# Performance work log

Hardware: AMD Instinct MI355X
Metric: run time of the kernel (lower is better)

## Reference

```python
import jax, jax.numpy as jnp
import numpy as np

B, G, S, GS, P = 32, 512, 128, 32, 10
C, H, RED = 384, 6, 16
HID = 4 * C
D = C // H
SCALE = D ** -0.5

def _gelu(x):
    return jax.nn.gelu(x, approximate=False)

def _ln(x, g, b):
    m = jnp.mean(x, -1, keepdims=True)
    v = jnp.var(x, -1, keepdims=True)
    return (x - m) * jax.lax.rsqrt(v + 1e-5) * g + b

def _split_qkv(x, W):
    Bn, T, Cc = x.shape
    qkv = (x @ W).reshape(Bn, T, 3, H, D).transpose(2, 0, 3, 1, 4)
    return qkv[0], qkv[1], qkv[2]

def _merge(x):
    Bn, Hh, T, Dd = x.shape
    return x.transpose(0, 2, 1, 3).reshape(Bn, T, Hh * Dd)

def _mha(q, k, v):
    a = jax.nn.softmax(jnp.einsum('bhnd,bhmd->bhnm', q, k) * SCALE, axis=-1)
    return jnp.einsum('bhnm,bhmd->bhnd', a, v)

def _forward(x, center1, center2, neighborhood, prompt_embeddings, ln1_g, ln1_b, Wqkv, Wproj, bproj, gate, ln2_g, ln2_b, W1, b1, W2, b2, ad_down_W, ad_down_b, ad_up_W, ad_up_b, ad_gate, bn_g, bn_b, bn_mean, bn_var, ln3_g, ln3_b, a1_Wqkv, a1_Wproj, a1_bproj, ad1_down_W, ad1_down_b, ad1_up_W, ad1_up_b, idx, center_idx, group_size, if_maxmean, pro_cof, center_cof):
    Bx, Ntok, Cc = x.shape
    # prompt dropout is identity in eval
    prompt = jnp.broadcast_to(prompt_embeddings, (Bx, P, Cc))
    # --- gated dual self / prompt-cross attention ---
    xn = _ln(x, ln1_g, ln1_b)
    q, k, v = _split_qkv(xn, Wqkv)
    xs = _mha(q, k, v)                                  # [B,H,N,D]
    _, pk, pv = _split_qkv(prompt, Wqkv)
    pa = jax.nn.softmax(jnp.einsum('bhnd,bhpd->bhnp', q, pk) * SCALE, axis=-1)
    px = jnp.einsum('bhnp,bhpd->bhnd', gate * pa, pv)   # learned gate per head
    x = x + (_merge(xs) + _merge(px)) @ Wproj + bproj
    # --- MLP + gated bottleneck adapter residual ---
    h = _gelu(_ln(x, ln2_g, ln2_b) @ W1 + b1) @ W2 + b2
    h_ad = h + _gelu(h @ ad_down_W + ad_down_b) @ ad_up_W + ad_up_b
    x = ad_gate * h_ad + x
    cls_x = x[:, :1]
    xt = x[:, 1:]                                       # [B,G,C]
    flat = xt.reshape(Bx * G, Cc)
    x_nb = flat[idx].reshape(Bx * S, group_size, Cc)    # KNN neighborhoods
    x_ct = flat[center_idx].reshape(Bx, S, Cc)          # center features
    # NOTE: original normalizes `neighborhood` by its std, but result is unused
    # --- local self-attention (attn1 over norm3) on each neighborhood ---
    nq, nk, nv = _split_qkv(_ln(x_nb, ln3_g, ln3_b), a1_Wqkv)
    no = _mha(nq, nk, nv)
    x_nb = x_nb + _merge(no) @ a1_Wproj + a1_bproj
    knn = x_nb.reshape(Bx, S, group_size, Cc)
    lc = jnp.max(knn, axis=2)
    if if_maxmean:
        lc = lc + jnp.mean(knn, axis=2)
    # BatchNorm1d (eval, running stats) + GELU over channel dim
    lc = _gelu((lc - bn_mean) * jax.lax.rsqrt(bn_var + 1e-5) * bn_g + bn_b)
    vis = lc + center_cof * x_ct                        # [B,S,C]
    # --- propagate: de_neighbors == S so sorted-topk == full weighted sum ---
    d = jnp.sum((center1[:, :, None, :] - center2[:, None, :, :]) ** 2, axis=-1)  # [B,G,S]
    w = 1.0 / (d + 1e-8)
    w = w / jnp.sum(w, axis=-1, keepdims=True)
    interp = jnp.einsum('bns,bsc->bnc', w, vis)
    xt = xt + pro_cof * interp
    out = jnp.concatenate([cls_x, xt], axis=1)
    # adapter1
    out = out + _gelu(out @ ad1_down_W + ad1_down_b) @ ad1_up_W + ad1_up_b
    return out

def setup_inputs():
    ks = jax.random.split(jax.random.key(0), 20)
    r = lambda i, shape, s=0.02: jax.random.normal(ks[i], shape, jnp.float32) * s
    return {
        'x': jax.random.normal(ks[0], (B, G + 1, C), jnp.float32),
        'center1': jax.random.normal(ks[1], (B, G, 3), jnp.float32),
        'center2': jax.random.normal(ks[2], (B, S, 3), jnp.float32),
        'neighborhood': jax.random.normal(ks[3], (B, S, GS, 3), jnp.float32),
        'prompt_embeddings': r(4, (P, C)),
        'ln1_g': jnp.ones(C), 'ln1_b': jnp.zeros(C),
        'Wqkv': r(5, (C, 3 * C)),
        'Wproj': r(6, (C, C)), 'bproj': jnp.zeros(C),
        'gate': jax.random.normal(ks[7], (1, H, 1, 1), jnp.float32),
        'ln2_g': jnp.ones(C), 'ln2_b': jnp.zeros(C),
        'W1': r(8, (C, HID)), 'b1': jnp.zeros(HID),
        'W2': r(9, (HID, C)), 'b2': jnp.zeros(C),
        'ad_down_W': r(10, (C, RED)), 'ad_down_b': jnp.zeros(RED),
        'ad_up_W': r(11, (RED, C)), 'ad_up_b': jnp.zeros(C),
        'ad_gate': jax.random.normal(ks[12], (), jnp.float32),
        'bn_g': jnp.ones(C), 'bn_b': jnp.zeros(C),
        'bn_mean': jnp.zeros(C), 'bn_var': jnp.ones(C),
        'ln3_g': jnp.ones(C), 'ln3_b': jnp.zeros(C),
        'a1_Wqkv': r(13, (C, 3 * C)),
        'a1_Wproj': r(14, (C, C)), 'a1_bproj': jnp.zeros(C),
        'ad1_down_W': r(15, (C, RED)), 'ad1_down_b': jnp.zeros(RED),
        'ad1_up_W': r(16, (RED, C)), 'ad1_up_b': jnp.zeros(C),
        'idx': jax.random.randint(ks[17], (B * S * GS,), 0, B * G),
        'center_idx': jax.random.randint(ks[18], (B * S,), 0, B * G),
        'group_size': GS,
        'if_maxmean': 1,
        'pro_cof': 1,
        'center_cof': 1,
    }

def reference(x, center1, center2, neighborhood, prompt_embeddings, ln1_g, ln1_b, Wqkv, Wproj, bproj, gate, ln2_g, ln2_b, W1, b1, W2, b2, ad_down_W, ad_down_b, ad_up_W, ad_up_b, ad_gate, bn_g, bn_b, bn_mean, bn_var, ln3_g, ln3_b, a1_Wqkv, a1_Wproj, a1_bproj, ad1_down_W, ad1_down_b, ad1_up_W, ad1_up_b, idx, center_idx, group_size, if_maxmean, pro_cof, center_cof):
    return _forward(x, center1, center2, neighborhood, prompt_embeddings, ln1_g, ln1_b, Wqkv, Wproj, bproj, gate, ln2_g, ln2_b, W1, b1, W2, b2, ad_down_W, ad_down_b, ad_up_W, ad_up_b, ad_gate, bn_g, bn_b, bn_mean, bn_var, ln3_g, ln3_b, a1_Wqkv, a1_Wproj, a1_bproj, ad1_down_W, ad1_down_b, ad1_up_W, ad1_up_b, idx, center_idx, group_size, if_maxmean, pro_cof, center_cof)
```

## Files before the change

kernel.cpp:

```cpp
#include <hip/hip_runtime.h>
#include <hip/hip_bf16.h>
#include <cstdint>
#include <cstddef>

typedef __hip_bfloat16 bf16;
constexpr int TOK = 32 * 513;

typedef __attribute__((ext_vector_type(8))) short short8;
typedef __attribute__((ext_vector_type(4))) float f32x4;

__device__ __forceinline__ float bflo(unsigned u){ return __uint_as_float(u << 16); }
__device__ __forceinline__ float bfhi(unsigned u){ return __uint_as_float(u & 0xffff0000u); }
__device__ __forceinline__ float b2f(bf16 x){ return __bfloat162float(x); }
__device__ __forceinline__ bf16  f2b(float x){ return __float2bfloat16(x); }
__device__ __forceinline__ float geluf(float x){ return 0.5f*x*(1.0f + erff(x*0.70710678118654752f)); }
__device__ __forceinline__ float scal(const int* p){
  const int i = *p;
  if (i > -1000000 && i < 1000000) return (float)i;
  return __int_as_float(i);
}
__device__ __forceinline__ f32x4 mfma16(short8 a, short8 b, f32x4 c){
  return __builtin_amdgcn_mfma_f32_16x16x32_bf16(a, b, c, 0, 0, 0);
}
__device__ __forceinline__ int swzl(int l){ return l ^ ((l >> 3) & 7); }
__device__ __forceinline__ void gload_lds16(const bf16* g, bf16* l){
  __builtin_amdgcn_global_load_lds(
      (const __attribute__((address_space(1))) void*)g,
      (__attribute__((address_space(3))) void*)l, 16, 0, 0);
}

__global__ __launch_bounds__(256) void detect_kernel(const unsigned* __restrict__ x,
                                                     int* __restrict__ flag)
{
  const int t = threadIdx.x;
  bool bad = false;
  for (int i = t; i < 2048; i += 256){
    const unsigned u = x[i];
    const float a = fabsf(bflo(u)), b = fabsf(bfhi(u));
    if (!(a < 1e6f) || !(b < 1e6f)) bad = true;
  }
  __shared__ int s;
  if (t == 0) s = 0;
  __syncthreads();
  const unsigned long long m = __ballot(bad);
  if (m != 0ull && (t & 63) == 0) atomicOr(&s, 1);
  __syncthreads();
  if (t == 0) *flag = s;
}

struct ConvArgs {
  const void* src[34];
  bf16*       dst[34];
  int         n[34];
};
__global__ __launch_bounds__(256) void convert_many(const int* __restrict__ flag, ConvArgs a)
{
  const int ii = blockIdx.y;
  const bool isf = (*flag != 0);
  const int n = a.n[ii];
  const int n8 = n >> 3;
  bf16* d = a.dst[ii];
  if (isf){
    const float4* s = (const float4*)a.src[ii];
    for (int i = blockIdx.x*256 + threadIdx.x; i < n8; i += gridDim.x*256){
      const float4 f0 = s[i*2];
      const float4 f1 = s[i*2 + 1];
      bf16 tmp[8] = {f2b(f0.x),f2b(f0.y),f2b(f0.z),f2b(f0.w),
                     f2b(f1.x),f2b(f1.y),f2b(f1.z),f2b(f1.w)};
      *(uint4*)(d + (size_t)i*8) = *(const uint4*)tmp;
    }
  } else {
    const uint4* s = (const uint4*)a.src[ii];
    for (int i = blockIdx.x*256 + threadIdx.x; i < n8; i += gridDim.x*256){
      ((uint4*)d)[i] = s[i];
    }
  }
  if (blockIdx.x == 0){
    for (int i = n8*8 + threadIdx.x; i < n; i += 256){
      d[i] = isf ? f2b(((const float*)a.src[ii])[i]) : ((const bf16*)a.src[ii])[i];
    }
  }
}

__global__ __launch_bounds__(256) void shuffle_b(const bf16* __restrict__ W,
    bf16* __restrict__ out, int N, int KT, int NT)
{
  const int id = blockIdx.x*256 + threadIdx.x;
  if (id >= NT*KT*64) return;
  const int l  = id & 63;
  const int k0 = (id >> 6) % KT;
  const int n0 = (id >> 6) / KT;
  bf16 tmp[8];
  #pragma unroll
  for (int j = 0; j < 8; j++)
    tmp[j] = W[(size_t)(k0*32 + (l>>4)*8 + j)*N + n0*16 + (l&15)];
  *(uint4*)(out + (size_t)id*8) = *(const uint4*)tmp;
}

template<bool SRC_BF16>
__global__ __launch_bounds__(256) void ln_kernel(const void* __restrict__ src,
    const bf16* __restrict__ g, const bf16* __restrict__ b,
    bf16* __restrict__ out, int rows)
{
  const int wave = (blockIdx.x * blockDim.x + threadIdx.x) >> 6;
  const int lane = threadIdx.x & 63;
  if (wave >= rows) return;
  float v[6]; float s = 0.f, s2 = 0.f;
  #pragma unroll
  for (int i = 0; i < 6; i++){
    const int c = lane + 64*i;
    float x;
    if (SRC_BF16) x = b2f(((const bf16*)src)[(size_t)wave*384 + c]);
    else          x = ((const float*)src)[(size_t)wave*384 + c];
    v[i] = x; s += x; s2 += x*x;
  }
  #pragma unroll
  for (int mm = 32; mm; mm >>= 1){ s += __shfl_xor(s, mm); s2 += __shfl_xor(s2, mm); }
  const float mean = s * (1.f/384.f);
  const float rs = rsqrtf(s2 * (1.f/384.f) - mean*mean + 1e-5f);
  #pragma unroll
  for (int i = 0; i < 6; i++){
    const int c = lane + 64*i;
    out[(size_t)wave*384 + c] = f2b((v[i]-mean)*rs*b2f(g[c]) + b2f(b[c]));
  }
}

template<int EPI>
__global__ __launch_bounds__(256) void mfma_gemm(
    const bf16* __restrict__ A, const bf16* __restrict__ Bsh,
    const bf16* __restrict__ bias, const bf16* __restrict__ resid,
    void* __restrict__ outv, int M, int N, int K)
{
  __shared__ __align__(16) bf16 sA[8*64*8];
  const int t = threadIdx.x, lane = t & 63, w = t >> 6;
  const int l15 = lane & 15, quad = lane >> 4;
  const int wm = w & 1, wn = w >> 1;
  const int m0 = blockIdx.y * 128;
  const int n0t = blockIdx.x * 8 + wn * 4;
  const int KT = K >> 5;
  f32x4 acc[4][4];
  #pragma unroll
  for (int i = 0; i < 4; i++){
    #pragma unroll
    for (int j = 0; j < 4; j++) acc[i][j] = f32x4{0.f,0.f,0.f,0.f};
  }
  const int mtA = 2*w, mtB = 2*w + 1;
  const bf16* gA = A + (size_t)(m0 + mtA*16 + l15)*K + quad*8;
  const bf16* gB = A + (size_t)(m0 + mtB*16 + l15)*K + quad*8;
  bf16* lA = sA + mtA*512;
  bf16* lB = sA + mtB*512;

  for (int ks = 0; ks < KT; ks++){
    gload_lds16(gA + ks*32, lA);
    gload_lds16(gB + ks*32, lB);
    __syncthreads();
    short8 afr[4];
    #pragma unroll
    for (int i = 0; i < 4; i++)
      afr[i] = *(const short8*)(sA + (((wm*4+i)*64 + lane) << 3));
    #pragma unroll
    for (int j = 0; j < 4; j++){
      const short8 b = *(const short8*)(Bsh + ((size_t)((n0t+j)*KT + ks)*64 + lane)*8);
      #pragma unroll
      for (int i = 0; i < 4; i++) acc[i][j] = mfma16(afr[i], b, acc[i][j]);
    }
    __syncthreads();
  }
  #pragma unroll
  for (int i = 0; i < 4; i++){
    #pragma unroll
    for (int r = 0; r < 4; r++){
      const int gm = m0 + (wm*4+i)*16 + quad*4 + r;
      if (gm < M){
        #pragma unroll
        for (int j = 0; j < 4; j++){
          const int gn = (n0t+j)*16 + l15;
          float v = acc[i][j][r];
          const size_t o = (size_t)gm*N + gn;
          if (EPI == 0){ v += b2f(bias[gn]); ((bf16*)outv)[o] = f2b(v); }
          else if (EPI == 1){ ((bf16*)outv)[o] = f2b(v); }
          else if (EPI == 2){ v += b2f(bias[gn]); ((bf16*)outv)[o] = f2b(geluf(v)); }
          else { v += b2f(bias[gn]) + b2f(resid[o]); ((float*)outv)[o] = v; }
        }
      }
    }
  }
}

__global__ __launch_bounds__(256) void pqkv_kernel(const bf16* __restrict__ pe,
    const bf16* __restrict__ Wqkv, float* __restrict__ pq)
{
  const int n  = blockIdx.x*64 + (threadIdx.x & 63);
  const int rg = threadIdx.x >> 6;
  for (int r = rg; r < 10; r += 4){
    float s0 = 0.f, s1 = 0.f;
    for (int c = 0; c < 384; c += 2){
      s0 = fmaf(b2f(pe[(size_t)r*384+c]),   b2f(Wqkv[(size_t)c*1152 + n]),     s0);
      s1 = fmaf(b2f(pe[(size_t)r*384+c+1]), b2f(Wqkv[(size_t)(c+1)*1152 + n]), s1);
    }
    pq[(size_t)r*1152 + n] = s0 + s1;
  }
}

__global__ __launch_bounds__(256) void attn_kernel(
    const bf16* __restrict__ qkv, const float* __restrict__ pq,
    const bf16* __restrict__ gate, bf16* __restrict__ ao)
{
  __shared__ __align__(16) bf16 s_vT[64*72];
  __shared__ __align__(16) bf16 s_p[4*16*40];
  __shared__ __align__(16) bf16 s_pk[16*72];
  __shared__ __align__(16) bf16 s_pvT[64*40];
  const int bh = blockIdx.y;
  const int b = bh / 6, h = bh % 6;
  const int q0 = blockIdx.x * 64;
  const int t = threadIdx.x, lane = t & 63, w = t >> 6;
  const int l15 = lane & 15, quad = lane >> 4;

  const int qtok = q0 + w*16 + l15;
  const int qtokc = qtok < 513 ? qtok : 512;
  const bf16* qp = qkv + (size_t)(b*513 + qtokc)*1152 + h*64 + quad*8;
  const short8 qf0 = *(const short8*)qp;
  const short8 qf1 = *(const short8*)(qp + 32);

  {
    const int j = t >> 4, dc = (t & 15) * 4;
    float f[4] = {0.f,0.f,0.f,0.f};
    if (j < 10){
      const float* pk = pq + (size_t)j*1152 + 384 + h*64 + dc;
      f[0]=pk[0]; f[1]=pk[1]; f[2]=pk[2]; f[3]=pk[3];
    }
    bf16 tmp[4] = {f2b(f[0]),f2b(f[1]),f2b(f[2]),f2b(f[3])};
    *(uint2*)(s_pk + j*72 + dc) = *(const uint2*)tmp;
  }
  {
    const int d = t & 63, kg = t >> 6;
    #pragma unroll
    for (int kk = 0; kk < 8; kk++){
      const int key = kg*8 + kk;
      bf16 v = f2b(0.f);
      if (key < 10) v = f2b(pq[(size_t)key*1152 + 768 + h*64 + d]);
      s_pvT[d*40 + key] = v;
    }
  }

  float m_i[4], l_i[4];
  f32x4 oacc[4];
  #pragma unroll
  for (int r = 0; r < 4; r++){ m_i[r] = -30000.f; l_i[r] = 0.f; }
  #pragma unroll
  for (int nt = 0; nt < 4; nt++) oacc[nt] = f32x4{0.f,0.f,0.f,0.f};
  bf16* myp = s_p + w*16*40;

  for (int kt = 0; kt < 9; kt++){
    const int kb = kt*64;
    __syncthreads();
    {
      const int kp = t & 31, dg = t >> 5;
      const int key0 = kb + 2*kp;
      uint4 v0 = {0,0,0,0}, v1 = {0,0,0,0};
      if (key0 < 513)
        v0 = *(const uint4*)(qkv + (size_t)(b*513 + key0)*1152 + 768 + h*64 + dg*8);
      if (key0 + 1 < 513)
        v1 = *(const uint4*)(qkv + (size_t)(b*513 + key0 + 1)*1152 + 768 + h*64 + dg*8);
      const unsigned short* a0 = (const unsigned short*)&v0;
      const unsigned short* a1 = (const unsigned short*)&v1;
      unsigned* vt = (unsigned*)s_vT;
      #pragma unroll
      for (int j = 0; j < 8; j++)
        vt[(dg*8 + j)*36 + kp] = (unsigned)a0[j] | ((unsigned)a1[j] << 16);
    }
    __syncthreads();

    f32x4 sreg[4];
    #pragma unroll
    for (int nt = 0; nt < 4; nt++){
      const int key = kb + nt*16 + l15;
      const int keyc = key < 513 ? key : 512;
      const bf16* kp2 = qkv + (size_t)(b*513 + keyc)*1152 + 384 + h*64 + quad*8;
      const short8 kf0 = *(const short8*)kp2;
      const short8 kf1 = *(const short8*)(kp2 + 32);
      f32x4 acc = mfma16(qf0, kf0, f32x4{0.f,0.f,0.f,0.f});
      acc = mfma16(qf1, kf1, acc);
      const bool kvalid = key < 513;
      #pragma unroll
      for (int r = 0; r < 4; r++)
        sreg[nt][r] = kvalid ? acc[r]*0.125f : -30000.f;
    }
    float alpha[4];
    #pragma unroll
    for (int r = 0; r < 4; r++){
      float mx = fmaxf(fmaxf(sreg[0][r], sreg[1][r]), fmaxf(sreg[2][r], sreg[3][r]));
      #pragma unroll
      for (int mm = 8; mm; mm >>= 1) mx = fmaxf(mx, __shfl_xor(mx, mm));
      const float mn = fmaxf(m_i[r], mx);
      alpha[r] = __expf(m_i[r] - mn);
      m_i[r] = mn;
      float ps = 0.f;
      #pragma unroll
      for (int nt = 0; nt < 4; nt++){
        const float p = __expf(sreg[nt][r] - mn);
        sreg[nt][r] = p; ps += p;
      }
      #pragma unroll
      for (int mm = 8; mm; mm >>= 1) ps += __shfl_xor(ps, mm);
      l_i[r] = l_i[r]*alpha[r] + ps;
    }
    #pragma unroll
    for (int nt = 0; nt < 4; nt++){
      #pragma unroll
      for (int r = 0; r < 4; r++)
        myp[(quad*4 + r)*40 + nt*16 + l15] = f2b(sreg[nt][r]);
    }
    #pragma unroll
    for (int nt = 0; nt < 4; nt++){
      #pragma unroll
      for (int r = 0; r < 4; r++) oacc[nt][r] *= alpha[r];
    }
    const short8* ap = (const short8*)(myp + l15*40);
    #pragma unroll
    for (int nt = 0; nt < 4; nt++){
      const short8* bv = (const short8*)(s_vT + (nt*16 + l15)*72);
      oacc[nt] = mfma16(ap[quad],     bv[quad],     oacc[nt]);
      oacc[nt] = mfma16(ap[4 + quad], bv[4 + quad], oacc[nt]);
    }
  }

  f32x4 sp;
  {
    f32x4 acc = f32x4{0.f,0.f,0.f,0.f};
    const short8* bp = (const short8*)(s_pk + l15*72);
    acc = mfma16(qf0, bp[quad],     acc);
    acc = mfma16(qf1, bp[4 + quad], acc);
    #pragma unroll
    for (int r = 0; r < 4; r++)
      sp[r] = (l15 < 10) ? acc[r]*0.125f : -30000.f;
  }
  float psr[4];
  #pragma unroll
  for (int r = 0; r < 4; r++){
    float mx = sp[r];
    #pragma unroll
    for (int mm = 8; mm; mm >>= 1) mx = fmaxf(mx, __shfl_xor(mx, mm));
    const float p = __expf(sp[r] - mx);
    float ps = p;
    #pragma unroll
    for (int mm = 8; mm; mm >>= 1) ps += __shfl_xor(ps, mm);
    psr[r] = ps;
    myp[(quad*4 + r)*40 + l15]      = f2b(p);
    myp[(quad*4 + r)*40 + 16 + l15] = f2b(0.f);
  }
  f32x4 pva[4];
  {
    const short8* ap = (const short8*)(myp + l15*40);
    #pragma unroll
    for (int nt = 0; nt < 4; nt++){
      const short8* bv = (const short8*)(s_pvT + (nt*16 + l15)*40);
      pva[nt] = mfma16(ap[quad], bv[quad], f32x4{0.f,0.f,0.f,0.f});
    }
  }

  const float gh = b2f(gate[h]);
  #pragma unroll
  for (int r = 0; r < 4; r++){
    const int tok = q0 + w*16 + quad*4 + r;
    if (tok < 513){
      const float invl = 1.f/l_i[r];
      const float gps  = gh/psr[r];
      #pragma unroll
      for (int nt = 0; nt < 4; nt++){
        const float val = oacc[nt][r]*invl + pva[nt][r]*gps;
        ao[(size_t)(b*513 + tok)*384 + h*64 + nt*16 + l15] = f2b(val);
      }
    }
  }
}

template<bool MID>
__global__ __launch_bounds__(256) void adapter_kernel(
    const void* __restrict__ src,
    const bf16* __restrict__ Wd, const bf16* __restrict__ bd,
    const bf16* __restrict__ Wu, const bf16* __restrict__ bu,
    const bf16* __restrict__ p_gate,
    const bf16* __restrict__ g3, const bf16* __restrict__ b3,
    const int* __restrict__ flag,
    float* __restrict__ xres, bf16* __restrict__ xln3,
    void* __restrict__ out)
{
  __shared__ float s_h[4][384];
  const int wv = threadIdx.x >> 6, lane = threadIdx.x & 63;
  const int row = blockIdx.x*4 + wv;
  float v[6];
  #pragma unroll
  for (int i = 0; i < 6; i++){
    const int c = lane + 64*i;
    float x;
    if (MID) x = b2f(((const bf16*)src)[(size_t)row*384 + c]);
    else     x = ((const float*)src)[(size_t)row*384 + c];
    v[i] = x; s_h[wv][c] = x;
  }
  const int o = lane & 15, p = lane >> 4;
  float part = 0.f;
  #pragma unroll 4
  for (int j = 0; j < 96; j++)
    part = fmaf(s_h[wv][p*96 + j], b2f(Wd[(size_t)(p*96 + j)*16 + o]), part);
  part += __shfl_xor(part, 16);
  part += __shfl_xor(part, 32);
  const float y = geluf(part + b2f(bd[o]));
  float up[6] = {0.f,0.f,0.f,0.f,0.f,0.f};
  #pragma unroll
  for (int o2 = 0; o2 < 16; o2++){
    const float yo = __shfl(y, o2);
    #pragma unroll
    for (int i = 0; i < 6; i++)
      up[i] = fmaf(yo, b2f(Wu[(size_t)o2*384 + lane + 64*i]), up[i]);
  }
  if (MID){
    const float g = b2f(p_gate[0]);
    float nv[6]; float s = 0.f, s2 = 0.f;
    #pragma unroll
    for (int i = 0; i < 6; i++){
      const int c = lane + 64*i;
      const float had = v[i] + up[i] + b2f(bu[c]);
      const float nx = g*had + xres[(size_t)row*384 + c];
      xres[(size_t)row*384 + c] = nx;
      nv[i] = nx; s += nx; s2 += nx*nx;
    }
    const int boff = row % 513;
    if (boff != 0){
      #pragma unroll
      for (int mm = 32; mm; mm >>= 1){ s += __shfl_xor(s, mm); s2 += __shfl_xor(s2, mm); }
      const float mean = s * (1.f/384.f);
      const float rs = rsqrtf(s2 * (1.f/384.f) - mean*mean + 1e-5f);
      const int r3 = (row/513)*512 + boff - 1;
      #pragma unroll
      for (int i = 0; i < 6; i++){
        const int c = lane + 64*i;
        xln3[(size_t)r3*384 + c] = f2b((nv[i]-mean)*rs*b2f(g3[c]) + b2f(b3[c]));
      }
    }
  } else {
    const bool isf = (*flag != 0);
    #pragma unroll
    for (int i = 0; i < 6; i++){
      const int c = lane + 64*i;
      const float ov = v[i] + up[i] + b2f(bu[c]);
      if (isf) ((float*)out)[(size_t)row*384 + c] = ov;
      else     ((bf16*)out)[(size_t)row*384 + c] = f2b(ov);
    }
  }
}

__global__ __launch_bounds__(512, 2) void local_kernel(
    const bf16* __restrict__ qkv3, const float* __restrict__ xres,
    const int* __restrict__ idx, const int* __restrict__ cidx,
    const bf16* __restrict__ Bp, const bf16* __restrict__ bp1,
    const bf16* __restrict__ bng, const bf16* __restrict__ bnb,
    const bf16* __restrict__ bnm, const bf16* __restrict__ bnv,
    const int* __restrict__ p_ifmm, const int* __restrict__ p_ccof,
    float* __restrict__ vis)
{
  __shared__ __align__(16) bf16 sV[3*4*64*8];
  __shared__ __align__(16) bf16 sP[3*2*64*8];
  __shared__ __align__(16) bf16 sO[3*4*64*8];
  __shared__ int s_flat[32];
  __shared__ int s_tok[32];

  const int g = blockIdx.x;
  const int t = threadIdx.x, lane = t & 63, w = t >> 6;
  const int l15 = lane & 15, quad = lane >> 4;
  const int lanez = swzl(lane);

  if (t < 32){
    const int r = idx[g*32 + t];
    s_flat[t] = r;
    s_tok[t]  = (r >> 9)*513 + 1 + (r & 511);
  }
  __syncthreads();

  const int vrowA = t & 31,          vccA = t >> 5;
  const int vrowB = (512 + t) & 31,  vccB = (512 + t) >> 5;
  const int vhA = vccA >> 3, vd0A = (vccA & 7) * 8;
  const int vhB = vccB >> 3, vd0B = (vccB & 7) * 8;
  const bool hasB = (t < 256);

  uint4 svA, svB;
  {
    svA = *(const uint4*)(qkv3 + (size_t)s_flat[vrowA]*1152 + 768 + (0*3 + vhA)*64 + vd0A);
    if (hasB) svB = *(const uint4*)(qkv3 + (size_t)s_flat[vrowB]*1152 + 768 + (0*3 + vhB)*64 + vd0B);
  }

  f32x4 accp[3][2];
  #pragma unroll
  for (int a = 0; a < 3; a++){
    #pragma unroll
    for (int m = 0; m < 2; m++) accp[a][m] = f32x4{0.f,0.f,0.f,0.f};
  }

  #pragma unroll
  for (int hc = 0; hc < 2; hc++){
    {
      const bf16* sa = (const bf16*)&svA;
      #pragma unroll
      for (int j2 = 0; j2 < 8; j2++){
        const int d = vd0A + j2;
        const int L = (vrowA>>3)*16 + (d&15);
        sV[((vhA*4 + (d>>4))*64 + swzl(L))*8 + (vrowA&7)] = sa[j2];
      }
      if (hasB){
        const bf16* sb = (const bf16*)&svB;
        #pragma unroll
        for (int j2 = 0; j2 < 8; j2++){
          const int d = vd0B + j2;
          const int L = (vrowB>>3)*16 + (d&15);
          sV[((vhB*4 + (d>>4))*64 + swzl(L))*8 + (vrowB&7)] = sb[j2];
        }
      }
    }
    __syncthreads();

    if (w < 6){
      const int h = w >> 1, mt = w & 1;
      const size_t qrow = (size_t)s_flat[mt*16 + l15]*1152;
      const int dcol = (hc*3 + h)*64 + quad*8;
      const short8 q0 = *(const short8*)(qkv3 + qrow + dcol);
      const short8 q1 = *(const short8*)(qkv3 + qrow + dcol + 32);
      f32x4 sr[2];
      #pragma unroll
      for (int nt = 0; nt < 2; nt++){
        const size_t krow = (size_t)s_flat[nt*16 + l15]*1152 + 384;
        const short8 k0 = *(const short8*)(qkv3 + krow + dcol);
        const short8 k1 = *(const short8*)(qkv3 + krow + dcol + 32);
        f32x4 acc = mfma16(q0, k0, f32x4{0.f,0.f,0.f,0.f});
        acc = mfma16(q1, k1, acc);
        #pragma unroll
        for (int r = 0; r < 4; r++) sr[nt][r] = acc[r]*0.125f;
      }
      #pragma unroll
      for (int r = 0; r < 4; r++){
        float mx = fmaxf(sr[0][r], sr[1][r]);
        #pragma unroll
        for (int mm = 8; mm; mm >>= 1) mx = fmaxf(mx, __shfl_xor(mx, mm));
        const float e0 = __expf(sr[0][r] - mx), e1 = __expf(sr[1][r] - mx);
        float sm = e0 + e1;
        #pragma unroll
        for (int mm = 8; mm; mm >>= 1) sm += __shfl_xor(sm, mm);
        const float inv = 1.f/sm;
        const int m = quad*4 + r;
        const int L0 = (l15 >> 3)*16       + m;
        const int L1 = (2 + (l15 >> 3))*16 + m;
        sP[((h*2 + mt)*64 + swzl(L0))*8 + (l15 & 7)] = f2b(e0*inv);
        sP[((h*2 + mt)*64 + swzl(L1))*8 + (l15 & 7)] = f2b(e1*inv);
      }
    }
    __syncthreads();

    {
      const int mt = w & 1, nt = w >> 1;
      const int k0w = nt >> 1, qdw = (nt & 1)*2 + (l15 >> 3), jw = l15 & 7;
      #pragma unroll
      for (int h = 0; h < 3; h++){
        const short8 a = *(const short8*)(sP + ((h*2 + mt)*64 + lanez)*8);
        const short8 b = *(const short8*)(sV + ((h*4 + nt)*64 + lanez)*8);
        const f32x4 o = mfma16(a, b, f32x4{0.f,0.f,0.f,0.f});
        #pragma unroll
        for (int r = 0; r < 4; r++){
          const int L = qdw*16 + quad*4 + r;
          sO[((h*4 + mt*2 + k0w)*64 + swzl(L))*8 + jw] = f2b(o[r]);
        }
      }
    }
    __syncthreads();

    if (hc == 0){
      svA = *(const uint4*)(qkv3 + (size_t)s_flat[vrowA]*1152 + 768 + (3 + vhA)*64 + vd0A);
      if (hasB) svB = *(const uint4*)(qkv3 + (size_t)s_flat[vrowB]*1152 + 768 + (3 + vhB)*64 + vd0B);
    }

    #pragma unroll
    for (int h = 0; h < 3; h++){
      short8 afr[2][2];
      #pragma unroll
      for (int mt = 0; mt < 2; mt++){
        #pragma unroll
        for (int k0l = 0; k0l < 2; k0l++)
          afr[mt][k0l] = *(const short8*)(sO + ((h*4 + mt*2 + k0l)*64 + lanez)*8);
      }
      const int hg2 = (hc*3 + h)*2;
      #pragma unroll
      for (int tt = 0; tt < 3; tt++){
        const int nt = w*3 + tt;
        #pragma unroll
        for (int k0l = 0; k0l < 2; k0l++){
          const short8 b = *(const short8*)(Bp + ((size_t)(nt*12 + hg2 + k0l)*64 + lane)*8);
          accp[tt][0] = mfma16(afr[0][k0l], b, accp[tt][0]);
          accp[tt][1] = mfma16(afr[1][k0l], b, accp[tt][1]);
        }
      }
    }
    __syncthreads();
  }

  const float fmm  = scal(p_ifmm);
  const float ccof = scal(p_ccof);
  const int cr = cidx[g];
  const int ctok = (cr >> 9)*513 + 1 + (cr & 511);
  #pragma unroll
  for (int tt = 0; tt < 3; tt++){
    const int n = (w*3 + tt)*16 + l15;
    const float bb = b2f(bp1[n]);
    float mx = -3e30f, sm = 0.f;
    #pragma unroll
    for (int mt = 0; mt < 2; mt++){
      #pragma unroll
      for (int r = 0; r < 4; r++){
        const int tok = mt*16 + quad*4 + r;
        const float v = accp[tt][mt][r] + bb + xres[(size_t)s_tok[tok]*384 + n];
        mx = fmaxf(mx, v); sm += v;
      }
    }
    mx = fmaxf(mx, __shfl_xor(mx, 16)); sm += __shfl_xor(sm, 16);
    mx = fmaxf(mx, __shfl_xor(mx, 32)); sm += __shfl_xor(sm, 32);
    if (quad == 0){
      const float lc = (fmm != 0.f) ? (mx + sm*(1.f/32.f)) : mx;
      const float nr = (lc - b2f(bnm[n])) * rsqrtf(b2f(bnv[n]) + 1e-5f) * b2f(bng[n]) + b2f(bnb[n]);
      vis[(size_t)g*384 + n] = geluf(nr) + ccof * xres[(size_t)ctok*384 + n];
    }
  }
}

__global__ __launch_bounds__(256) void interp_kernel(const bf16* __restrict__ c1,
    const bf16* __restrict__ c2, const float* __restrict__ vis,
    const int* __restrict__ p_pcof, float* __restrict__ xres)
{
  __shared__ float s_w[8][128];
  __shared__ float s_red[2];
  const int b = blockIdx.y;
  const int n0 = blockIdx.x * 8;
  const int t = threadIdx.x;
  for (int ni = 0; ni < 8; ni++){
    const int n = n0 + ni;
    float wv = 0.f;
    if (t < 128){
      float d2 = 0.f;
      #pragma unroll
      for (int k = 0; k < 3; k++){
        const float a = b2f(c1[((size_t)b*512 + n)*3 + k]);
        const float c = b2f(c2[((size_t)b*128 + t)*3 + k]);
        const float df = a - c; d2 += df*df;
      }
      wv = 1.f/(d2 + 1e-8f);
    }
    float rsum = wv;
    #pragma unroll
    for (int mm = 32; mm; mm >>= 1) rsum += __shfl_xor(rsum, mm);
    if (((t & 63) == 0) && t < 128) s_red[t >> 6] = rsum;
    __syncthreads();
    const float tot = s_red[0] + s_red[1];
    if (t < 128) s_w[ni][t] = wv / tot;
    __syncthreads();
  }
  float acc1[8], acc2[8];
  #pragma unroll
  for (int ni = 0; ni < 8; ni++){ acc1[ni] = 0.f; acc2[ni] = 0.f; }
  for (int s = 0; s < 128; s++){
    const float* vp = vis + ((size_t)b*128 + s)*384;
    const float v1 = vp[t];
    const float v2 = (t < 128) ? vp[t + 256] : 0.f;
    #pragma unroll
    for (int ni = 0; ni < 8; ni++){
      const float wn = s_w[ni][s];
      acc1[ni] = fmaf(wn, v1, acc1[ni]);
      acc2[ni] = fmaf(wn, v2, acc2[ni]);
    }
  }
  const float pc = scal(p_pcof);
  #pragma unroll
  for (int ni = 0; ni < 8; ni++){
    const int tok = b*513 + 1 + n0 + ni;
    xres[(size_t)tok*384 + t] += pc*acc1[ni];
    if (t < 128) xres[(size_t)tok*384 + t + 256] += pc*acc2[ni];
  }
}

extern "C" void kernel_launch(void* const* d_in, const int* in_sizes, int n_in,
                              void* d_out, int out_size, void* d_ws, size_t ws_size,
                              hipStream_t stream)
{
  (void)n_in; (void)out_size; (void)ws_size;
  const int*  idx   = (const int*)d_in[35];
  const int*  cidx  = (const int*)d_in[36];
  const int*  ifmm  = (const int*)d_in[38];
  const int*  pcof  = (const int*)d_in[39];
  const int*  ccof  = (const int*)d_in[40];

  size_t off = 0;
  auto alloc = [&](size_t bytes) -> void* {
    void* p = (char*)d_ws + off; off += (bytes + 255) & ~(size_t)255; return p;
  };
  int*   flag = (int*)  alloc(sizeof(int));
  float* xres = (float*)alloc((size_t)TOK*384*4);
  bf16*  slab = (bf16*) alloc((size_t)TOK*1536*2);
  bf16*  xn   = (bf16*) alloc((size_t)TOK*384*2);
  float* pq   = (float*)alloc((size_t)10*1152*4);
  bf16*  Bq   = (bf16*) alloc((size_t)72*12*64*8*2);
  bf16*  Bp   = (bf16*) alloc((size_t)24*12*64*8*2);
  bf16*  Bqkv = (bf16*) alloc((size_t)72*12*64*8*2);
  bf16*  Bw1  = (bf16*) alloc((size_t)96*12*64*8*2);
  bf16*  Bw2  = (bf16*) alloc((size_t)24*48*64*8*2);
  bf16*  Bwp  = (bf16*) alloc((size_t)24*12*64*8*2);

  bf16*  qkvb = slab;
  bf16*  x_c  = slab + (size_t)TOK*1152;
  bf16*  h1   = slab;
  bf16*  qkv3 = slab;
  bf16*  xln3 = slab + (size_t)TOK*1152;
  bf16*  ao   = xn;
  bf16*  hbuf = xn;
  float* visb = (float*)xn;

  const int conv_ids[34] = {0,1,2,4,5,6,7,8,9,10,11,12,13,14,15,16,17,
                            18,19,20,21,22,23,24,25,26,27,28,29,30,31,32,33,34};
  ConvArgs ca;
  bf16* canon[41];
  int maxn = 1;
  for (int k = 0; k < 34; k++){
    const int i = conv_ids[k];
    const int n = in_sizes[i];
    bf16* dst = (i == 0) ? x_c : (bf16*)alloc((size_t)n*2);
    ca.src[k] = d_in[i]; ca.dst[k] = dst; ca.n[k] = n;
    canon[i] = dst;
    if (n > maxn) maxn = n;
  }
  detect_kernel<<<dim3(1), dim3(256), 0, stream>>>((const unsigned*)d_in[0], flag);
  {
    int gx = (maxn/8 + 255) / 256; if (gx > 512) gx = 512; if (gx < 1) gx = 1;
    convert_many<<<dim3(gx, 34), dim3(256), 0, stream>>>(flag, ca);
  }

  const bf16 *x_in = canon[0], *c1 = canon[1], *c2 = canon[2], *pe = canon[4],
             *ln1g = canon[5], *ln1b = canon[6], *Wqkv = canon[7], *Wproj = canon[8],
             *bproj = canon[9], *gate = canon[10], *ln2g = canon[11], *ln2b = canon[12],
             *W1 = canon[13], *b1 = canon[14], *W2 = canon[15], *b2v = canon[16],
             *adW = canon[17], *adb = canon[18], *adU = canon[19], *adub = canon[20],
             *adg = canon[21], *bng = canon[22], *bnb = canon[23], *bnm = canon[24],
             *bnv = canon[25], *ln3g = canon[26], *ln3b = canon[27], *a1W = canon[28],
             *a1P = canon[29], *a1pb = canon[30], *d1W = canon[31], *d1b = canon[32],
             *u1W = canon[33], *u1b = canon[34];

  shuffle_b<<<dim3(216), dim3(256), 0, stream>>>(a1W, Bq, 1152, 12, 72);
  shuffle_b<<<dim3(72),  dim3(256), 0, stream>>>(a1P, Bp, 384, 12, 24);
  shuffle_b<<<dim3(216), dim3(256), 0, stream>>>(Wqkv, Bqkv, 1152, 12, 72);
  shuffle_b<<<dim3(288), dim3(256), 0, stream>>>(W1, Bw1, 1536, 12, 96);
  shuffle_b<<<dim3(288), dim3(256), 0, stream>>>(W2, Bw2, 384, 48, 24);
  shuffle_b<<<dim3(72),  dim3(256), 0, stream>>>(Wproj, Bwp, 384, 12, 24);

  ln_kernel<true><<<dim3((TOK*64)/256), dim3(256), 0, stream>>>((const void*)x_in, ln1g, ln1b, xn, TOK);
  mfma_gemm<1><<<dim3(9,129), dim3(256), 0, stream>>>(xn, Bqkv, nullptr, nullptr, qkvb, TOK, 1152, 384);
  pqkv_kernel<<<dim3(18), dim3(256), 0, stream>>>(pe, Wqkv, pq);
  attn_kernel<<<dim3(9,192), dim3(256), 0, stream>>>(qkvb, pq, gate, ao);
  mfma_gemm<3><<<dim3(3,129), dim3(256), 0, stream>>>(ao, Bwp, bproj, x_in, xres, TOK, 384, 384);
  ln_kernel<false><<<dim3((TOK*64)/256), dim3(256), 0, stream>>>((const void*)xres, ln2g, ln2b, xn, TOK);
  mfma_gemm<2><<<dim3(12,129), dim3(256), 0, stream>>>(xn, Bw1, b1, nullptr, h1, TOK, 1536, 384);
  mfma_gemm<0><<<dim3(3,129), dim3(256), 0, stream>>>(h1, Bw2, b2v, nullptr, hbuf, TOK, 384, 1536);
  adapter_kernel<true><<<dim3(TOK/4), dim3(256), 0, stream>>>(
      (const void*)hbuf, adW, adb, adU, adub, adg, ln3g, ln3b, nullptr, xres, xln3, nullptr);
  mfma_gemm<1><<<dim3(9,128), dim3(256), 0, stream>>>(xln3, Bq, nullptr, nullptr, qkv3, 16384, 1152, 384);
  local_kernel<<<dim3(4096), dim3(512), 0, stream>>>(qkv3, xres, idx, cidx, Bp, a1pb,
                                                     bng, bnb, bnm, bnv, ifmm, ccof, visb);
  interp_kernel<<<dim3(64,32), dim3(256), 0, stream>>>(c1, c2, visb, pcof, xres);
  adapter_kernel<false><<<dim3(TOK/4), dim3(256), 0, stream>>>(
      (const void*)xres, d1W, d1b, u1W, u1b, nullptr, nullptr, nullptr, flag, nullptr, nullptr, d_out);
}
```

Before: 802.5 us.

## Double-buffer K tiles via async LDS loads in attention and batch weight shuffles

The attention kernel now prefetches the next K tile into a double-buffered shared-memory array using async global-to-LDS loads, and register-prefetches the next V tile, so global latency overlaps the softmax and PV work of the current tile. The P scratch stride changes from 40 to 64. Separately, the six weight-shuffle launches are merged into one multi-tensor launch to cut launch overhead. This adds shared memory, which may reduce occupancy, and the stride-64 P layout may cause LDS bank conflicts.

Result: faster. 783.3 us (-2.4%).

```diff
diff --git a/kernel.cpp b/kernel.cpp
--- a/kernel.cpp
+++ b/kernel.cpp
@@ -82,19 +82,28 @@
   }
 }
 
-__global__ __launch_bounds__(256) void shuffle_b(const bf16* __restrict__ W,
-    bf16* __restrict__ out, int N, int KT, int NT)
-{
+struct ShufArgs {
+  const bf16* W[6];
+  bf16*       out[6];
+  int         N[6];
+  int         KT[6];
+  int         NT[6];
+};
+__global__ __launch_bounds__(256) void shuffle_many(ShufArgs a)
+{
+  const int ii = blockIdx.y;
   const int id = blockIdx.x*256 + threadIdx.x;
+  const int KT = a.KT[ii], NT = a.NT[ii], N = a.N[ii];
   if (id >= NT*KT*64) return;
   const int l  = id & 63;
   const int k0 = (id >> 6) % KT;
   const int n0 = (id >> 6) / KT;
+  const bf16* W = a.W[ii];
   bf16 tmp[8];
   #pragma unroll
   for (int j = 0; j < 8; j++)
     tmp[j] = W[(size_t)(k0*32 + (l>>4)*8 + j)*N + n0*16 + (l&15)];
-  *(uint4*)(out + (size_t)id*8) = *(const uint4*)tmp;
+  *(uint4*)(a.out[ii] + (size_t)id*8) = *(const uint4*)tmp;
 }
 
 template<bool SRC_BF16>
@@ -206,8 +215,9 @@
     const bf16* __restrict__ qkv, const float* __restrict__ pq,
     const bf16* __restrict__ gate, bf16* __restrict__ ao)
 {
+  __shared__ __align__(16) bf16 s_kf[2][8*64*8];
   __shared__ __align__(16) bf16 s_vT[64*72];
-  __shared__ __align__(16) bf16 s_p[4*16*40];
+  __shared__ __align__(16) bf16 s_p[4*16*64];
   __shared__ __align__(16) bf16 s_pk[16*72];
   __shared__ __align__(16) bf16 s_pvT[64*40];
   const int bh = blockIdx.y;
@@ -222,6 +232,16 @@
   const short8 qf0 = *(const short8*)qp;
   const short8 qf1 = *(const short8*)(qp + 32);
 
+  auto issueK = [&](int kb, int buf){
+    const int key = kb + w*16 + l15;
+    const int keyc = key < 513 ? key : 512;
+    const bf16* src = qkv + (size_t)(b*513 + keyc)*1152 + 384 + h*64 + quad*8;
+    gload_lds16(src,      &s_kf[buf][((w*2 + 0)*64)*8]);
+    gload_lds16(src + 32, &s_kf[buf][((w*2 + 1)*64)*8]);
+  };
+
+  const int kp = t & 31, dg = t >> 5;
+
   {
     const int j = t >> 4, dc = (t & 15) * 4;
     float f[4] = {0.f,0.f,0.f,0.f};
@@ -243,27 +263,31 @@
     }
   }
 
+  uint4 pv0 = {0,0,0,0}, pv1 = {0,0,0,0};
+  {
+    const int key0 = 2*kp;
+    if (key0 < 513)
+      pv0 = *(const uint4*)(qkv + (size_t)(b*513 + key0)*1152 + 768 + h*64 + dg*8);
+    if (key0 + 1 < 513)
+      pv1 = *(const uint4*)(qkv + (size_t)(b*513 + key0 + 1)*1152 + 768 + h*64 + dg*8);
+  }
+  issueK(0, 0);
+  int cur = 0;
+
   float m_i[4], l_i[4];
   f32x4 oacc[4];
   #pragma unroll
   for (int r = 0; r < 4; r++){ m_i[r] = -30000.f; l_i[r] = 0.f; }
   #pragma unroll
   for (int nt = 0; nt < 4; nt++) oacc[nt] = f32x4{0.f,0.f,0.f,0.f};
-  bf16* myp = s_p + w*16*40;
+  bf16* myp = s_p + w*16*64;
 
   for (int kt = 0; kt < 9; kt++){
     const int kb = kt*64;
     __syncthreads();
     {
-      const int kp = t & 31, dg = t >> 5;
-      const int key0 = kb + 2*kp;
-      uint4 v0 = {0,0,0,0}, v1 = {0,0,0,0};
-      if (key0 < 513)
-        v0 = *(const uint4*)(qkv + (size_t)(b*513 + key0)*1152 + 768 + h*64 + dg*8);
-      if (key0 + 1 < 513)
-        v1 = *(const uint4*)(qkv + (size_t)(b*513 + key0 + 1)*1152 + 768 + h*64 + dg*8);
-      const unsigned short* a0 = (const unsigned short*)&v0;
-      const unsigned short* a1 = (const unsigned short*)&v1;
+      const unsigned short* a0 = (const unsigned short*)&pv0;
+      const unsigned short* a1 = (const unsigned short*)&pv1;
       unsigned* vt = (unsigned*)s_vT;
       #pragma unroll
       for (int j = 0; j < 8; j++)
@@ -274,18 +298,26 @@
     f32x4 sreg[4];
     #pragma unroll
     for (int nt = 0; nt < 4; nt++){
-      const int key = kb + nt*16 + l15;
-      const int keyc = key < 513 ? key : 512;
-      const bf16* kp2 = qkv + (size_t)(b*513 + keyc)*1152 + 384 + h*64 + quad*8;
-      const short8 kf0 = *(const short8*)kp2;
-      const short8 kf1 = *(const short8*)(kp2 + 32);
+      const short8 kf0 = *(const short8*)(&s_kf[cur][((nt*2 + 0)*64 + lane)*8]);
+      const short8 kf1 = *(const short8*)(&s_kf[cur][((nt*2 + 1)*64 + lane)*8]);
       f32x4 acc = mfma16(qf0, kf0, f32x4{0.f,0.f,0.f,0.f});
       acc = mfma16(qf1, kf1, acc);
-      const bool kvalid = key < 513;
+      const bool kvalid = (kb + nt*16 + l15) < 513;
       #pragma unroll
       for (int r = 0; r < 4; r++)
         sreg[nt][r] = kvalid ? acc[r]*0.125f : -30000.f;
     }
+
+    if (kt < 8){
+      issueK(kb + 64, cur ^ 1);
+      const int key0 = kb + 64 + 2*kp;
+      pv0 = {0,0,0,0}; pv1 = {0,0,0,0};
+      if (key0 < 513)
+        pv0 = *(const uint4*)(qkv + (size_t)(b*513 + key0)*1152 + 768 + h*64 + dg*8);
+      if (key0 + 1 < 513)
+        pv1 = *(const uint4*)(qkv + (size_t)(b*513 + key0 + 1)*1152 + 768 + h*64 + dg*8);
+    }
+
     float alpha[4];
     #pragma unroll
     for (int r = 0; r < 4; r++){
@@ -309,20 +341,21 @@
     for (int nt = 0; nt < 4; nt++){
       #pragma unroll
       for (int r = 0; r < 4; r++)
-        myp[(quad*4 + r)*40 + nt*16 + l15] = f2b(sreg[nt][r]);
+        myp[(quad*4 + r)*64 + nt*16 + l15] = f2b(sreg[nt][r]);
     }
     #pragma unroll
     for (int nt = 0; nt < 4; nt++){
       #pragma unroll
       for (int r = 0; r < 4; r++) oacc[nt][r] *= alpha[r];
     }
-    const short8* ap = (const short8*)(myp + l15*40);
+    const short8* ap = (const short8*)(myp + l15*64);
     #pragma unroll
     for (int nt = 0; nt < 4; nt++){
       const short8* bv = (const short8*)(s_vT + (nt*16 + l15)*72);
       oacc[nt] = mfma16(ap[quad],     bv[quad],     oacc[nt]);
       oacc[nt] = mfma16(ap[4 + quad], bv[4 + quad], oacc[nt]);
     }
+    cur ^= 1;
   }
 
   f32x4 sp;
@@ -346,12 +379,12 @@
     #pragma unroll
     for (int mm = 8; mm; mm >>= 1) ps += __shfl_xor(ps, mm);
     psr[r] = ps;
-    myp[(quad*4 + r)*40 + l15]      = f2b(p);
-    myp[(quad*4 + r)*40 + 16 + l15] = f2b(0.f);
+    myp[(quad*4 + r)*64 + l15]      = f2b(p);
+    myp[(quad*4 + r)*64 + 16 + l15] = f2b(0.f);
   }
   f32x4 pva[4];
   {
-    const short8* ap = (const short8*)(myp + l15*40);
+    const short8* ap = (const short8*)(myp + l15*64);
     #pragma unroll
     for (int nt = 0; nt < 4; nt++){
       const short8* bv = (const short8*)(s_pvT + (nt*16 + l15)*40);
@@ -747,12 +780,16 @@
              *a1P = canon[29], *a1pb = canon[30], *d1W = canon[31], *d1b = canon[32],
              *u1W = canon[33], *u1b = canon[34];
 
-  shuffle_b<<<dim3(216), dim3(256), 0, stream>>>(a1W, Bq, 1152, 12, 72);
-  shuffle_b<<<dim3(72),  dim3(256), 0, stream>>>(a1P, Bp, 384, 12, 24);
-  shuffle_b<<<dim3(216), dim3(256), 0, stream>>>(Wqkv, Bqkv, 1152, 12, 72);
-  shuffle_b<<<dim3(288), dim3(256), 0, stream>>>(W1, Bw1, 1536, 12, 96);
-  shuffle_b<<<dim3(288), dim3(256), 0, stream>>>(W2, Bw2, 384, 48, 24);
-  shuffle_b<<<dim3(72),  dim3(256), 0, stream>>>(Wproj, Bwp, 384, 12, 24);
+  {
+    ShufArgs sa;
+    sa.W[0]=a1W;   sa.out[0]=Bq;   sa.N[0]=1152; sa.KT[0]=12; sa.NT[0]=72;
+    sa.W[1]=a1P;   sa.out[1]=Bp;   sa.N[1]=384;  sa.KT[1]=12; sa.NT[1]=24;
+    sa.W[2]=Wqkv;  sa.out[2]=Bqkv; sa.N[2]=1152; sa.KT[2]=12; sa.NT[2]=72;
+    sa.W[3]=W1;    sa.out[3]=Bw1;  sa.N[3]=1536; sa.KT[3]=12; sa.NT[3]=96;
+    sa.W[4]=W2;    sa.out[4]=Bw2;  sa.N[4]=384;  sa.KT[4]=48; sa.NT[4]=24;
+    sa.W[5]=Wproj; sa.out[5]=Bwp;  sa.N[5]=384;  sa.KT[5]=12; sa.NT[5]=24;
+    shuffle_many<<<dim3(288, 6), dim3(256), 0, stream>>>(sa);
+  }
 
   ln_kernel<true><<<dim3((TOK*64)/256), dim3(256), 0, stream>>>((const void*)x_in, ln1g, ln1b, xn, TOK);
   mfma_gemm<1><<<dim3(9,129), dim3(256), 0, stream>>>(xn, Bqkv, nullptr, nullptr, qkvb, TOK, 1152, 384);
```
